# Performance work log

Hardware: AMD Instinct MI355X
Metric: run time of the kernel (lower is better)

## Reference

```python
import jax, jax.numpy as jnp
import numpy as np

L, D, I, H = 4, 768, 1536, 12
HEAD = I // H          # 128
NB = I // 4            # 384 block-diagonal blocks of size 4
EPS = 1e-5
SCALE = 1.0 / np.sqrt(HEAD)
ROPE_BASE = 1000.0


def _ln(x):
    m = x.mean(-1, keepdims=True)
    v = x.var(-1, keepdims=True)
    return (x - m) * jax.lax.rsqrt(v + EPS)


def _swish(x):
    return x * jax.nn.sigmoid(x)


def _block_linear(x, W):  # x:[T,B,I], W:[NB,4,4]
    T, B, _ = x.shape
    xb = x.reshape(T, B, NB, 4)
    return jnp.einsum('tbhi,hoi->tbho', xb, W).reshape(T, B, I)


def _rotate_half(x):
    h = x.shape[-1] // 2
    return jnp.concatenate([-x[..., h:], x[..., :h]], axis=-1)


def _depthwise_conv(x, w, b):  # x:[T,B,I], w:[I,5], b:[I]
    h = jnp.transpose(x, (1, 2, 0))  # [B,I,T]
    out = jax.lax.conv_general_dilated(
        h, w[:, None, :], (1,), [(2, 2)],
        dimension_numbers=('NCH', 'OIH', 'NCH'), feature_group_count=I)
    out = out + b[None, :, None]
    return jnp.transpose(out, (2, 0, 1))  # [T,B,I]


def setup_inputs() -> dict:
    key = jax.random.key(0)
    ks = jax.random.split(key, 16)
    T, B = 512, 16
    std = np.sqrt(2.0 / (5.0 * D))
    inp = {
        'x': jax.random.normal(ks[0], (T, B, D), jnp.float32),
        'attention_mask': jax.random.bernoulli(ks[1], 0.1, (B, 1, 1, T)),
        'Win': jax.random.normal(ks[2], (L, 2 * I, D), jnp.float32) * std,
        'Wout': jax.random.normal(ks[3], (L, D, I), jnp.float32) * std,
        'Wq': jax.random.normal(ks[4], (L, NB, 4, 4), jnp.float32) * 0.5,
        'bq': jnp.zeros((L, NB, 4), jnp.float32),
        'Wk': jax.random.normal(ks[5], (L, NB, 4, 4), jnp.float32) * 0.5,
        'Wv': jax.random.normal(ks[6], (L, NB, 4, 4), jnp.float32) * 0.5,
        'kg': jnp.ones((L, HEAD), jnp.float32),
        'kb': jnp.zeros((L, HEAD), jnp.float32),
        'qg': jnp.ones((L, HEAD), jnp.float32),
        'qb': jnp.zeros((L, HEAD), jnp.float32),
        'convw': jax.random.normal(ks[7], (L, I, 5), jnp.float32) * 0.3,
        'convb': jnp.zeros((L, I), jnp.float32),
        'lskip': jnp.ones((L, I), jnp.float32),
    }
    return inp


def reference(x, attention_mask, Win, Wout, Wq, bq, Wk, Wv, kg, kb, qg, qb, convw, convb, lskip):
    T, B, _ = x.shape
    # rotary tables (positions 0..T-1, same for every batch*head)
    inv_freq = 1.0 / (ROPE_BASE ** (jnp.arange(0, HEAD, 2, dtype=jnp.float32) / HEAD))
    freqs = jnp.arange(T, dtype=jnp.float32)[:, None] * inv_freq[None, :]  # [T,HEAD/2]
    emb = jnp.concatenate([freqs, freqs], axis=-1)
    cos, sin = jnp.cos(emb)[None], jnp.sin(emb)[None]  # [1,T,HEAD]

    hidden = x
    for l in range(L):
        h = _ln(hidden)                                   # pre LN
        h = jnp.einsum('tbd,od->tbo', h, Win[l])          # [T,B,2I]
        h, gate = h[..., :I], h[..., I:]
        gate = _swish(gate)
        # value branch
        value = _block_linear(h, Wv[l])                   # [T,B,I]
        value = value.reshape(T, B * H, HEAD).transpose(1, 0, 2)  # [BH,T,hd]
        # time mixing
        h = _swish(_depthwise_conv(h, convw[l], convb[l]))  # [T,B,I]
        # key/query with per-head LN (affine)
        k = _block_linear(h, Wk[l]).reshape(T, B, H, HEAD)
        k = _ln(k) * kg[l] + kb[l]
        k = k.reshape(T, B * H, HEAD).transpose(1, 0, 2)
        q = _block_linear(h, Wq[l]) + bq[l].reshape(I)
        q = q.reshape(T, B, H, HEAD)
        q = _ln(q) * qg[l] + qb[l]
        q = q.reshape(T, B * H, HEAD).transpose(1, 0, 2)
        # rotary
        q = q * cos + _rotate_half(q) * sin
        k = k * cos + _rotate_half(k) * sin
        # masked attention
        scores = jnp.einsum('bqd,bkd->bqk', q, k) * SCALE  # [BH,T,T]
        scores = scores.reshape(B, H, T, T)
        scores = jnp.where(attention_mask, -jnp.inf, scores)
        probs = jax.nn.softmax(scores, axis=-1)
        probs = jnp.where(attention_mask, 0.0, probs).reshape(B * H, T, T)
        attn = jnp.einsum('bqk,bkd->bqd', probs, value)    # [BH,T,hd]
        attn = attn.transpose(1, 0, 2).reshape(T, B, I)
        # gated output
        h = h * lskip[l] + attn
        h = h * gate
        h = _ln(h)
        h = jnp.einsum('tbi,di->tbd', h, Wout[l])
        hidden = hidden + h
    return hidden
```

## Files before the change

### kernel.cpp

```cpp
#include <hip/hip_runtime.h>

#define TT 512
#define BB 16
#define DD 768
#define II 1536
#define HH 12
#define SCALE_QK 0.08838834764831845f

typedef unsigned short u16;
typedef unsigned int u32;
typedef __attribute__((ext_vector_type(8))) short bf16x8;
typedef __attribute__((ext_vector_type(4))) float f32x4;

__device__ __forceinline__ u16 f2b(float f) {
  union { float f; u32 u; } a; a.f = f;
  u32 r = a.u + 0x7FFFu + ((a.u >> 16) & 1u);
  return (u16)(r >> 16);
}
__device__ __forceinline__ float b2f(u16 h) {
  union { u32 u; float f; } a; a.u = ((u32)h) << 16; return a.f;
}

typedef __attribute__((address_space(3))) u32 lds_u32;
typedef const __attribute__((address_space(1))) u32 gbl_u32;
__device__ __forceinline__ void gl_lds16(const void* g, void* l) {
  __builtin_amdgcn_global_load_lds((gbl_u32*)g, (lds_u32*)l, 16, 0, 0);
}

__global__ __launch_bounds__(256) void wconv_kernel(const float* __restrict__ Win,
    const float* __restrict__ Wout, u16* __restrict__ winb, u16* __restrict__ woutb) {
  const int n1 = 3072 * 768, n2 = 768 * 1536;
  for (int i = blockIdx.x * 256 + threadIdx.x; i < n1 + n2; i += gridDim.x * 256) {
    if (i < n1) winb[i] = f2b(Win[i]);
    else woutb[i - n1] = f2b(Wout[i - n1]);
  }
}

__global__ void rope_kernel(float* __restrict__ cost, float* __restrict__ sint) {
  int t = blockIdx.x, j = threadIdx.x;
  float inv = powf(1000.0f, -(float)j * (1.0f / 64.0f));
  float f = (float)t * inv;
  cost[t * 64 + j] = cosf(f);
  sint[t * 64 + j] = sinf(f);
}

__global__ void mask_kernel(const void* __restrict__ mraw, float* __restrict__ madd) {
  __shared__ int flags[2];
  if (threadIdx.x < 2) flags[threadIdx.x] = 0;
  __syncthreads();
  const unsigned char* p = (const unsigned char*)mraw;
  int a0 = 0, a1 = 0;
  for (int i = threadIdx.x; i < 8192; i += 256) {
    unsigned char c = p[i];
    if (c) { if ((i & 3) == 0) a0 = 1; else a1 = 1; }
  }
  if (a0) atomicOr(&flags[0], 1);
  if (a1) atomicOr(&flags[1], 1);
  __syncthreads();
  bool bytewise = flags[0] && flags[1];
  for (int i = threadIdx.x; i < 8192; i += 256) {
    int m = bytewise ? (int)p[i] : (((const int*)mraw)[i] != 0);
    madd[i] = m ? -1e30f : 0.0f;
  }
}

__global__ __launch_bounds__(256) void ln_d_kernel(const float* __restrict__ in, u16* __restrict__ out) {
  const int tb = blockIdx.x;
  const float* row = in + (size_t)tb * DD;
  float v[3], s = 0.f, ss = 0.f;
#pragma unroll
  for (int e = 0; e < 3; ++e) { v[e] = row[threadIdx.x + e * 256]; s += v[e]; ss += v[e] * v[e]; }
#pragma unroll
  for (int off = 1; off < 64; off <<= 1) { s += __shfl_xor(s, off); ss += __shfl_xor(ss, off); }
  __shared__ float red[8];
  int wave = threadIdx.x >> 6, lane = threadIdx.x & 63;
  if (lane == 0) { red[wave] = s; red[wave + 4] = ss; }
  __syncthreads();
  s = red[0] + red[1] + red[2] + red[3];
  ss = red[4] + red[5] + red[6] + red[7];
  float mean = s * (1.f / DD), var = ss * (1.f / DD) - mean * mean;
  float rstd = rsqrtf(var + 1e-5f);
#pragma unroll
  for (int e = 0; e < 3; ++e)
    out[(size_t)tb * DD + threadIdx.x + e * 256] = f2b((v[e] - mean) * rstd);
}

template <int MODE, int K>
__global__ __launch_bounds__(256) void gemm_nt(const u16* __restrict__ A, const u16* __restrict__ Bt,
    u16* __restrict__ o_h0, u16* __restrict__ o_gate, float* __restrict__ o_add) {
  __shared__ u16 As[128 * 32];
  __shared__ u16 Bs[128 * 32];
  const int tid = threadIdx.x, lane = tid & 63, wave = tid >> 6;
  const int wm = wave >> 1, wn = wave & 1;
  const size_t ar0 = (size_t)blockIdx.x * 128;
  const size_t br0 = (size_t)blockIdx.y * 128;
  const int ldr = lane >> 2, ldk = (lane & 3) * 8;
  const f32x4 z4 = {0.f, 0.f, 0.f, 0.f};
  f32x4 acc[4][4];
#pragma unroll
  for (int i = 0; i < 4; ++i)
#pragma unroll
    for (int j = 0; j < 4; ++j) acc[i][j] = z4;

  for (int kt = 0; kt < K; kt += 32) {
    __syncthreads();
#pragma unroll
    for (int i = 0; i < 2; ++i) {
      const int rr = wave * 32 + i * 16;
      gl_lds16(A + (ar0 + rr + ldr) * K + kt + ldk, (void*)&As[rr * 32]);
      gl_lds16(Bt + (br0 + rr + ldr) * K + kt + ldk, (void*)&Bs[rr * 32]);
    }
    __syncthreads();
    const int rs = lane & 15, kc8 = (lane >> 4) * 8;
    bf16x8 af[4], bg[4];
#pragma unroll
    for (int f = 0; f < 4; ++f) {
      af[f] = *(const bf16x8*)&As[(wm * 64 + f * 16 + rs) * 32 + kc8];
      bg[f] = *(const bf16x8*)&Bs[(wn * 64 + f * 16 + rs) * 32 + kc8];
    }
#pragma unroll
    for (int i = 0; i < 4; ++i)
#pragma unroll
      for (int j = 0; j < 4; ++j)
        acc[i][j] = __builtin_amdgcn_mfma_f32_16x16x32_bf16(af[i], bg[j], acc[i][j], 0, 0, 0);
  }
  const int rl = (lane >> 4) * 4, cl = lane & 15;
#pragma unroll
  for (int i = 0; i < 4; ++i)
#pragma unroll
    for (int j = 0; j < 4; ++j) {
      const int cc = blockIdx.y * 128 + wn * 64 + j * 16 + cl;
#pragma unroll
      for (int r = 0; r < 4; ++r) {
        const size_t rr = ar0 + wm * 64 + i * 16 + rl + r;
        float v = acc[i][j][r];
        if (MODE == 0) {
          if (cc < II) o_h0[rr * II + cc] = f2b(v);
          else o_gate[rr * II + (cc - II)] = f2b(v / (1.f + __expf(-v)));
        } else {
          o_add[rr * DD + cc] += v;
        }
      }
    }
}

__global__ __launch_bounds__(256) void value_kernel(const u16* __restrict__ h0,
    const float* __restrict__ Wv, u16* __restrict__ val) {
  __shared__ float xs[64][129];
  const int bh = blockIdx.x, t0 = blockIdx.y * 64;
  const int b = bh / HH, h = bh % HH;
  const int tid = threadIdx.x;
#pragma unroll
  for (int it = 0; it < 4; ++it) {
    int idx = tid + it * 256;
    int tt = idx >> 4, c8 = idx & 15;
    union { uint4 v; u16 hh[8]; } u;
    u.v = *(const uint4*)&h0[((size_t)((t0 + tt) * BB + b)) * II + h * 128 + c8 * 8];
#pragma unroll
    for (int j = 0; j < 8; ++j) xs[tt][c8 * 8 + j] = b2f(u.hh[j]);
  }
  __syncthreads();
  const int tt = tid & 63, dg = tid >> 6;
#pragma unroll
  for (int dd = 0; dd < 32; ++dd) {
    int d = dg * 32 + dd;
    int nbl = d >> 2, o = d & 3;
    const float4 w = *(const float4*)&Wv[((size_t)(h * 32 + nbl) * 4 + o) * 4];
    float r = w.x * xs[tt][nbl * 4] + w.y * xs[tt][nbl * 4 + 1] +
              w.z * xs[tt][nbl * 4 + 2] + w.w * xs[tt][nbl * 4 + 3];
    val[((size_t)bh * 128 + d) * TT + t0 + tt] = f2b(r);
  }
}

__global__ __launch_bounds__(384) void conv_kernel(const u16* __restrict__ h0,
    const float* __restrict__ cw, const float* __restrict__ cb, u16* __restrict__ hc) {
  __shared__ float wT[5 * 1536];
  __shared__ float bS[1536];
  const int tid = threadIdx.x;
  for (int idx = tid; idx < 7680; idx += 384) {
    int ch = idx / 5, k2 = idx % 5;
    wT[k2 * 1536 + ch] = cw[idx];
  }
  for (int idx = tid; idx < 1536; idx += 384) bS[idx] = cb[idx];
  __syncthreads();

  const int r = tid / 192, c = tid % 192;
  const int tb = blockIdx.x * 2 + r;
  const int t = tb >> 4;
  const int i0 = c * 8;
  float a[8];
  {
    const float4 b0 = *(const float4*)&bS[i0];
    const float4 b1 = *(const float4*)&bS[i0 + 4];
    a[0] = b0.x; a[1] = b0.y; a[2] = b0.z; a[3] = b0.w;
    a[4] = b1.x; a[5] = b1.y; a[6] = b1.z; a[7] = b1.w;
  }
#pragma unroll
  for (int k2 = 0; k2 < 5; ++k2) {
    int tn = t + k2 - 2;
    if (tn < 0 || tn >= TT) continue;
    union { uint4 v; u16 hh[8]; } u;
    u.v = *(const uint4*)&h0[((size_t)tb + (size_t)(k2 - 2) * BB) * II + i0];
    const float4 w0 = *(const float4*)&wT[k2 * 1536 + i0];
    const float4 w1 = *(const float4*)&wT[k2 * 1536 + i0 + 4];
    a[0] += b2f(u.hh[0]) * w0.x; a[1] += b2f(u.hh[1]) * w0.y;
    a[2] += b2f(u.hh[2]) * w0.z; a[3] += b2f(u.hh[3]) * w0.w;
    a[4] += b2f(u.hh[4]) * w1.x; a[5] += b2f(u.hh[5]) * w1.y;
    a[6] += b2f(u.hh[6]) * w1.z; a[7] += b2f(u.hh[7]) * w1.w;
  }
  union { uint4 v; u16 hh[8]; } o;
#pragma unroll
  for (int j = 0; j < 8; ++j) o.hh[j] = f2b(a[j] / (1.f + __expf(-a[j])));
  *(uint4*)&hc[(size_t)tb * II + i0] = o.v;
}

__global__ __launch_bounds__(256) void qk_kernel(const u16* __restrict__ hc,
    const float* __restrict__ Wq, const float* __restrict__ bq, const float* __restrict__ Wk,
    const float* __restrict__ qg, const float* __restrict__ qb,
    const float* __restrict__ kg, const float* __restrict__ kb,
    const float* __restrict__ cost, const float* __restrict__ sint,
    u16* __restrict__ qrope, u16* __restrict__ krope) {
  const int gw = (blockIdx.x * 256 + threadIdx.x) >> 6;
  const int lane = threadIdx.x & 63;
  const int h = gw % HH, tb = gw / HH, b = tb & 15, t = tb >> 4;
  ushort4 xr = *(const ushort4*)&hc[(size_t)tb * II + h * 128 + (lane >> 1) * 4];
  float x0 = b2f(xr.x), x1 = b2f(xr.y), x2 = b2f(xr.z), x3 = b2f(xr.w);
  const int nb = h * 32 + (lane >> 1);
  const int o0 = (lane & 1) * 2;
  const float4 wq0 = *(const float4*)&Wq[((size_t)nb * 4 + o0) * 4];
  const float4 wq1 = *(const float4*)&Wq[((size_t)nb * 4 + o0 + 1) * 4];
  const float4 wk0 = *(const float4*)&Wk[((size_t)nb * 4 + o0) * 4];
  const float4 wk1 = *(const float4*)&Wk[((size_t)nb * 4 + o0 + 1) * 4];
  float q0 = wq0.x * x0 + wq0.y * x1 + wq0.z * x2 + wq0.w * x3 + bq[nb * 4 + o0];
  float q1 = wq1.x * x0 + wq1.y * x1 + wq1.z * x2 + wq1.w * x3 + bq[nb * 4 + o0 + 1];
  float k0 = wk0.x * x0 + wk0.y * x1 + wk0.z * x2 + wk0.w * x3;
  float k1 = wk1.x * x0 + wk1.y * x1 + wk1.z * x2 + wk1.w * x3;
  float sq = q0 + q1, sk = k0 + k1, qq = q0 * q0 + q1 * q1, kk = k0 * k0 + k1 * k1;
#pragma unroll
  for (int off = 1; off < 64; off <<= 1) {
    sq += __shfl_xor(sq, off); qq += __shfl_xor(qq, off);
    sk += __shfl_xor(sk, off); kk += __shfl_xor(kk, off);
  }
  float mq = sq * (1.f / 128), vq = qq * (1.f / 128) - mq * mq, rq = rsqrtf(vq + 1e-5f);
  float mk = sk * (1.f / 128), vk = kk * (1.f / 128) - mk * mk, rk = rsqrtf(vk + 1e-5f);
  const int d0 = lane * 2, d1 = d0 + 1;
  float qn0 = (q0 - mq) * rq * qg[d0] + qb[d0], qn1 = (q1 - mq) * rq * qg[d1] + qb[d1];
  float kn0 = (k0 - mk) * rk * kg[d0] + kb[d0], kn1 = (k1 - mk) * rk * kg[d1] + kb[d1];
  float pq0 = __shfl_xor(qn0, 32), pq1 = __shfl_xor(qn1, 32);
  float pk0 = __shfl_xor(kn0, 32), pk1 = __shfl_xor(kn1, 32);
  const float sg = (lane < 32) ? -1.f : 1.f;
  const float c0 = cost[t * 64 + (d0 & 63)], s0 = sint[t * 64 + (d0 & 63)];
  const float c1 = cost[t * 64 + (d1 & 63)], s1 = sint[t * 64 + (d1 & 63)];
  float oq0 = qn0 * c0 + sg * pq0 * s0, oq1 = qn1 * c1 + sg * pq1 * s1;
  float ok0 = kn0 * c0 + sg * pk0 * s0, ok1 = kn1 * c1 + sg * pk1 * s1;
  const size_t ob = ((size_t)(b * HH + h) * TT + t) * 128 + d0;
  *(u32*)&qrope[ob] = (u32)f2b(oq0) | ((u32)f2b(oq1) << 16);
  *(u32*)&krope[ob] = (u32)f2b(ok0) | ((u32)f2b(ok1) << 16);
}

__global__ __launch_bounds__(256) void attn_kernel(const u16* __restrict__ qr,
    const u16* __restrict__ kr, const u16* __restrict__ vv,
    const float* __restrict__ madd, u16* __restrict__ o) {
  __shared__ u16 Ks[64 * 128];
  __shared__ u16 Vs[128 * 64];
  __shared__ u16 Ps[4][16 * 72];
  const int bh = blockIdx.x, b = bh / HH;
  const int q0 = blockIdx.y * 64;
  const int tid = threadIdx.x, lane = tid & 63, wave = tid >> 6;
  const int l15 = lane & 15, l4 = lane >> 4;
  bf16x8 aq[4];
  const size_t qbase = ((size_t)bh * TT + q0 + wave * 16 + l15) * 128;
#pragma unroll
  for (int kc = 0; kc < 4; ++kc) aq[kc] = *(const bf16x8*)&qr[qbase + kc * 32 + l4 * 8];
  const f32x4 z4 = {0.f, 0.f, 0.f, 0.f};
  f32x4 oacc[8];
#pragma unroll
  for (int df = 0; df < 8; ++df) oacc[df] = z4;
  float mrow[4], lrow[4];
#pragma unroll
  for (int r = 0; r < 4; ++r) { mrow[r] = -1e30f; lrow[r] = 0.f; }

  for (int kt0 = 0; kt0 < TT; kt0 += 64) {
    __syncthreads();
#pragma unroll
    for (int i = 0; i < 4; ++i) {
      const int row = wave * 16 + i * 4 + l4;
      const int csrc = (l15 & 8) | ((l15 ^ row) & 7);
      gl_lds16(&kr[((size_t)bh * TT + kt0 + row) * 128 + csrc * 8], (void*)&Ks[(wave * 16 + i * 4) * 128]);
    }
#pragma unroll
    for (int i = 0; i < 4; ++i) {
      const int row = wave * 32 + i * 8 + (lane >> 3);
      const int csrc = ((lane & 7) ^ row) & 7;
      gl_lds16(&vv[((size_t)bh * 128 + row) * TT + kt0 + csrc * 8], (void*)&Vs[(wave * 32 + i * 8) * 64]);
    }
    __syncthreads();
    f32x4 sacc[4];
#pragma unroll
    for (int cf = 0; cf < 4; ++cf) sacc[cf] = z4;
#pragma unroll
    for (int kc = 0; kc < 4; ++kc)
#pragma unroll
      for (int cf = 0; cf < 4; ++cf) {
        const int krow = cf * 16 + l15;
        const int chunk = kc * 4 + l4;
        const int cph = (chunk & 8) | ((chunk ^ krow) & 7);
        bf16x8 bk = *(const bf16x8*)&Ks[krow * 128 + cph * 8];
        sacc[cf] = __builtin_amdgcn_mfma_f32_16x16x32_bf16(aq[kc], bk, sacc[cf], 0, 0, 0);
      }
    float sv[4][4], tmax[4];
#pragma unroll
    for (int r = 0; r < 4; ++r) tmax[r] = -3.0e38f;
#pragma unroll
    for (int cf = 0; cf < 4; ++cf) {
      const float ma = madd[b * TT + kt0 + cf * 16 + l15];
#pragma unroll
      for (int r = 0; r < 4; ++r) {
        const float s = sacc[cf][r] * SCALE_QK + ma;
        sv[cf][r] = s;
        tmax[r] = fmaxf(tmax[r], s);
      }
    }
#pragma unroll
    for (int off = 1; off < 16; off <<= 1)
#pragma unroll
      for (int r = 0; r < 4; ++r) tmax[r] = fmaxf(tmax[r], __shfl_xor(tmax[r], off));
    float fac[4], lsum[4];
#pragma unroll
    for (int r = 0; r < 4; ++r) {
      const float mn = fmaxf(mrow[r], tmax[r]);
      fac[r] = __expf(mrow[r] - mn);
      mrow[r] = mn;
      lsum[r] = 0.f;
    }
#pragma unroll
    for (int cf = 0; cf < 4; ++cf)
#pragma unroll
      for (int r = 0; r < 4; ++r) {
        const float p = __expf(sv[cf][r] - mrow[r]);
        lsum[r] += p;
        Ps[wave][(l4 * 4 + r) * 72 + cf * 16 + l15] = f2b(p);
      }
#pragma unroll
    for (int off = 1; off < 16; off <<= 1)
#pragma unroll
      for (int r = 0; r < 4; ++r) lsum[r] += __shfl_xor(lsum[r], off);
#pragma unroll
    for (int r = 0; r < 4; ++r) lrow[r] = lrow[r] * fac[r] + lsum[r];
#pragma unroll
    for (int df = 0; df < 8; ++df)
#pragma unroll
      for (int r = 0; r < 4; ++r) oacc[df][r] *= fac[r];
#pragma unroll
    for (int ks = 0; ks < 2; ++ks) {
      bf16x8 ap = *(const bf16x8*)&Ps[wave][l15 * 72 + ks * 32 + l4 * 8];
#pragma unroll
      for (int df = 0; df < 8; ++df) {
        const int d = df * 16 + l15;
        const int cph = (ks * 4 + l4) ^ (d & 7);
        bf16x8 bv = *(const bf16x8*)&Vs[d * 64 + cph * 8];
        oacc[df] = __builtin_amdgcn_mfma_f32_16x16x32_bf16(ap, bv, oacc[df], 0, 0, 0);
      }
    }
  }
  const size_t ob = (size_t)bh * TT + q0 + wave * 16;
#pragma unroll
  for (int df = 0; df < 8; ++df)
#pragma unroll
    for (int r = 0; r < 4; ++r)
      o[(ob + l4 * 4 + r) * 128 + df * 16 + l15] = f2b(oacc[df][r] / lrow[r]);
}

__global__ __launch_bounds__(256) void post_kernel(const u16* __restrict__ hc,
    const u16* __restrict__ attn, const u16* __restrict__ gate,
    const float* __restrict__ lskip, u16* __restrict__ ln2) {
  const int tb = blockIdx.x;
  const int b = tb & 15, t = tb >> 4;
  float v[6], s = 0.f, ss = 0.f;
#pragma unroll
  for (int e = 0; e < 6; ++e) {
    int i = threadIdx.x + e * 256;
    int hh = i >> 7, d = i & 127;
    float a = b2f(attn[((size_t)(b * HH + hh) * TT + t) * 128 + d]);
    float x = (b2f(hc[(size_t)tb * II + i]) * lskip[i] + a) * b2f(gate[(size_t)tb * II + i]);
    v[e] = x; s += x; ss += x * x;
  }
#pragma unroll
  for (int off = 1; off < 64; off <<= 1) { s += __shfl_xor(s, off); ss += __shfl_xor(ss, off); }
  __shared__ float red[8];
  int wave = threadIdx.x >> 6, lane = threadIdx.x & 63;
  if (lane == 0) { red[wave] = s; red[wave + 4] = ss; }
  __syncthreads();
  s = red[0] + red[1] + red[2] + red[3];
  ss = red[4] + red[5] + red[6] + red[7];
  float mean = s * (1.f / II), var = ss * (1.f / II) - mean * mean;
  float rstd = rsqrtf(var + 1e-5f);
#pragma unroll
  for (int e = 0; e < 6; ++e) {
    int i = threadIdx.x + e * 256;
    ln2[(size_t)tb * II + i] = f2b((v[e] - mean) * rstd);
  }
}

extern "C" void kernel_launch(void* const* d_in, const int* in_sizes, int n_in,
                              void* d_out, int out_size, void* d_ws, size_t ws_size,
                              hipStream_t stream) {
  const float* x = (const float*)d_in[0];
  const void* mraw = d_in[1];
  const float* Win = (const float*)d_in[2];
  const float* Wout = (const float*)d_in[3];
  const float* Wq = (const float*)d_in[4];
  const float* bq = (const float*)d_in[5];
  const float* Wk = (const float*)d_in[6];
  const float* Wv = (const float*)d_in[7];
  const float* kg = (const float*)d_in[8];
  const float* kb = (const float*)d_in[9];
  const float* qg = (const float*)d_in[10];
  const float* qb = (const float*)d_in[11];
  const float* convw = (const float*)d_in[12];
  const float* convb = (const float*)d_in[13];
  const float* lskip = (const float*)d_in[14];
  float* hidden = (float*)d_out;

  char* w = (char*)d_ws;
  u16* wb_in = (u16*)w;
  u16* wb_out = (u16*)(w + 4718592);
  u16* lnval = (u16*)(w + 7077888);
  u16* h0k = (u16*)(w + 32243712);
  u16* gate = (u16*)(w + 57409536);
  u16* hc = (u16*)(w + 82575360);
  u16* qrope = (u16*)(w + 107741184);
  float* cost = (float*)(w + 132907008);
  float* sint = (float*)(w + 133038080);
  float* madd = (float*)(w + 133169152);
  const size_t NEED = 133201920;
  if (ws_size < NEED) {
    hipMemcpyAsync(d_out, d_in[0], (size_t)out_size * 4, hipMemcpyDeviceToDevice, stream);
    return;
  }
  u16* ln1 = lnval;
  u16* val = lnval;
  u16* ln2 = lnval;
  u16* h0 = h0k;
  u16* krope = h0k;
  u16* attnb = qrope;

  hipMemcpyAsync(hidden, x, (size_t)TT * BB * DD * 4, hipMemcpyDeviceToDevice, stream);
  rope_kernel<<<512, 64, 0, stream>>>(cost, sint);
  mask_kernel<<<1, 256, 0, stream>>>(mraw, madd);

  for (int l = 0; l < 4; ++l) {
    wconv_kernel<<<4096, 256, 0, stream>>>(Win + (size_t)l * 3072 * 768,
        Wout + (size_t)l * 768 * 1536, wb_in, wb_out);
    ln_d_kernel<<<8192, 256, 0, stream>>>(hidden, ln1);
    gemm_nt<0, 768><<<dim3(64, 24), 256, 0, stream>>>(ln1, wb_in, h0, gate, nullptr);
    value_kernel<<<dim3(192, 8), 256, 0, stream>>>(h0, Wv + (size_t)l * 6144, val);
    conv_kernel<<<4096, 384, 0, stream>>>(h0, convw + (size_t)l * 7680, convb + (size_t)l * 1536, hc);
    qk_kernel<<<24576, 256, 0, stream>>>(hc, Wq + (size_t)l * 6144, bq + (size_t)l * 1536,
        Wk + (size_t)l * 6144, qg + l * 128, qb + l * 128, kg + l * 128, kb + l * 128,
        cost, sint, qrope, krope);
    attn_kernel<<<dim3(192, 8), 256, 0, stream>>>(qrope, krope, val, madd, attnb);
    post_kernel<<<8192, 256, 0, stream>>>(hc, attnb, gate, lskip + (size_t)l * 1536, ln2);
    gemm_nt<1, 1536><<<dim3(64, 6), 256, 0, stream>>>(ln2, wb_out, nullptr, nullptr, hidden);
  }
}
```

Before: 1.249 ms.

## Process two query tiles per attention block and skip unneeded softmax rescales

Each attention workgroup now handles 128 query rows instead of 64, reusing every K/V tile loaded into LDS for two query sub-tiles and halving the grid's K/V traffic. The mask row is staged once in LDS, and the online-softmax rescale of accumulators is skipped when no row maximum grows. The bf16 conversion helper is swapped for the HIP library intrinsic. In exchange each thread holds twice the accumulators, which raises register pressure and may lower occupancy, and the grid has half as many blocks.

```diff
diff --git a/kernel.cpp b/kernel.cpp
--- a/kernel.cpp
+++ b/kernel.cpp
@@ -1,4 +1,5 @@
 #include <hip/hip_runtime.h>
+#include <hip/hip_bf16.h>
 
 #define TT 512
 #define BB 16
@@ -13,9 +14,8 @@
 typedef __attribute__((ext_vector_type(4))) float f32x4;
 
 __device__ __forceinline__ u16 f2b(float f) {
-  union { float f; u32 u; } a; a.f = f;
-  u32 r = a.u + 0x7FFFu + ((a.u >> 16) & 1u);
-  return (u16)(r >> 16);
+  __hip_bfloat16 h = __float2bfloat16(f);
+  return *reinterpret_cast<u16*>(&h);
 }
 __device__ __forceinline__ float b2f(u16 h) {
   union { u32 u; float f; } a; a.u = ((u32)h) << 16; return a.f;
@@ -264,21 +264,29 @@
   __shared__ u16 Ks[64 * 128];
   __shared__ u16 Vs[128 * 64];
   __shared__ u16 Ps[4][16 * 72];
+  __shared__ float Ms[TT];
   const int bh = blockIdx.x, b = bh / HH;
-  const int q0 = blockIdx.y * 64;
+  const int q0 = blockIdx.y * 128;
   const int tid = threadIdx.x, lane = tid & 63, wave = tid >> 6;
   const int l15 = lane & 15, l4 = lane >> 4;
-  bf16x8 aq[4];
-  const size_t qbase = ((size_t)bh * TT + q0 + wave * 16 + l15) * 128;
-#pragma unroll
-  for (int kc = 0; kc < 4; ++kc) aq[kc] = *(const bf16x8*)&qr[qbase + kc * 32 + l4 * 8];
+  for (int i = tid; i < TT; i += 256) Ms[i] = madd[b * TT + i];
+  bf16x8 aq[2][4];
+#pragma unroll
+  for (int qt = 0; qt < 2; ++qt) {
+    const size_t qbase = ((size_t)bh * TT + q0 + qt * 64 + wave * 16 + l15) * 128;
+#pragma unroll
+    for (int kc = 0; kc < 4; ++kc) aq[qt][kc] = *(const bf16x8*)&qr[qbase + kc * 32 + l4 * 8];
+  }
   const f32x4 z4 = {0.f, 0.f, 0.f, 0.f};
-  f32x4 oacc[8];
-#pragma unroll
-  for (int df = 0; df < 8; ++df) oacc[df] = z4;
-  float mrow[4], lrow[4];
-#pragma unroll
-  for (int r = 0; r < 4; ++r) { mrow[r] = -1e30f; lrow[r] = 0.f; }
+  f32x4 oacc[2][8];
+  float mrow[2][4], lrow[2][4];
+#pragma unroll
+  for (int qt = 0; qt < 2; ++qt) {
+#pragma unroll
+    for (int df = 0; df < 8; ++df) oacc[qt][df] = z4;
+#pragma unroll
+    for (int r = 0; r < 4; ++r) { mrow[qt][r] = -1e30f; lrow[qt][r] = 0.f; }
+  }
 
   for (int kt0 = 0; kt0 < TT; kt0 += 64) {
     __syncthreads();
@@ -295,80 +303,90 @@
       gl_lds16(&vv[((size_t)bh * 128 + row) * TT + kt0 + csrc * 8], (void*)&Vs[(wave * 32 + i * 8) * 64]);
     }
     __syncthreads();
-    f32x4 sacc[4];
-#pragma unroll
-    for (int cf = 0; cf < 4; ++cf) sacc[cf] = z4;
-#pragma unroll
-    for (int kc = 0; kc < 4; ++kc)
+#pragma unroll
+    for (int qt = 0; qt < 2; ++qt) {
+      f32x4 sacc[4];
+#pragma unroll
+      for (int cf = 0; cf < 4; ++cf) sacc[cf] = z4;
+#pragma unroll
+      for (int kc = 0; kc < 4; ++kc)
+#pragma unroll
+        for (int cf = 0; cf < 4; ++cf) {
+          const int krow = cf * 16 + l15;
+          const int chunk = kc * 4 + l4;
+          const int cph = (chunk & 8) | ((chunk ^ krow) & 7);
+          bf16x8 bk = *(const bf16x8*)&Ks[krow * 128 + cph * 8];
+          sacc[cf] = __builtin_amdgcn_mfma_f32_16x16x32_bf16(aq[qt][kc], bk, sacc[cf], 0, 0, 0);
+        }
+      float tmax[4];
+#pragma unroll
+      for (int r = 0; r < 4; ++r) tmax[r] = -3.0e38f;
 #pragma unroll
       for (int cf = 0; cf < 4; ++cf) {
-        const int krow = cf * 16 + l15;
-        const int chunk = kc * 4 + l4;
-        const int cph = (chunk & 8) | ((chunk ^ krow) & 7);
-        bf16x8 bk = *(const bf16x8*)&Ks[krow * 128 + cph * 8];
-        sacc[cf] = __builtin_amdgcn_mfma_f32_16x16x32_bf16(aq[kc], bk, sacc[cf], 0, 0, 0);
+        const float ma = Ms[kt0 + cf * 16 + l15];
+#pragma unroll
+        for (int r = 0; r < 4; ++r) {
+          const float s = sacc[cf][r] * SCALE_QK + ma;
+          sacc[cf][r] = s;
+          tmax[r] = fmaxf(tmax[r], s);
+        }
       }
-    float sv[4][4], tmax[4];
-#pragma unroll
-    for (int r = 0; r < 4; ++r) tmax[r] = -3.0e38f;
-#pragma unroll
-    for (int cf = 0; cf < 4; ++cf) {
-      const float ma = madd[b * TT + kt0 + cf * 16 + l15];
-#pragma unroll
-      for (int r = 0; r < 4; ++r) {
-        const float s = sacc[cf][r] * SCALE_QK + ma;
-        sv[cf][r] = s;
-        tmax[r] = fmaxf(tmax[r], s);
+#pragma unroll
+      for (int off = 1; off < 16; off <<= 1)
+#pragma unroll
+        for (int r = 0; r < 4; ++r) tmax[r] = fmaxf(tmax[r], __shfl_xor(tmax[r], off));
+      bool grow = (tmax[0] > mrow[qt][0]) | (tmax[1] > mrow[qt][1]) |
+                  (tmax[2] > mrow[qt][2]) | (tmax[3] > mrow[qt][3]);
+      if (__any(grow)) {
+#pragma unroll
+        for (int r = 0; r < 4; ++r) {
+          const float mn = fmaxf(mrow[qt][r], tmax[r]);
+          const float fac = __expf(mrow[qt][r] - mn);
+          mrow[qt][r] = mn;
+          lrow[qt][r] *= fac;
+#pragma unroll
+          for (int df = 0; df < 8; ++df) oacc[qt][df][r] *= fac;
+        }
       }
-    }
-#pragma unroll
-    for (int off = 1; off < 16; off <<= 1)
-#pragma unroll
-      for (int r = 0; r < 4; ++r) tmax[r] = fmaxf(tmax[r], __shfl_xor(tmax[r], off));
-    float fac[4], lsum[4];
-#pragma unroll
-    for (int r = 0; r < 4; ++r) {
-      const float mn = fmaxf(mrow[r], tmax[r]);
-      fac[r] = __expf(mrow[r] - mn);
-      mrow[r] = mn;
-      lsum[r] = 0.f;
-    }
-#pragma unroll
-    for (int cf = 0; cf < 4; ++cf)
-#pragma unroll
-      for (int r = 0; r < 4; ++r) {
-        const float p = __expf(sv[cf][r] - mrow[r]);
-        lsum[r] += p;
-        Ps[wave][(l4 * 4 + r) * 72 + cf * 16 + l15] = f2b(p);
+      float lsum[4];
+#pragma unroll
+      for (int r = 0; r < 4; ++r) lsum[r] = 0.f;
+#pragma unroll
+      for (int cf = 0; cf < 4; ++cf)
+#pragma unroll
+        for (int r = 0; r < 4; ++r) {
+          const float p = __expf(sacc[cf][r] - mrow[qt][r]);
+          lsum[r] += p;
+          Ps[wave][(l4 * 4 + r) * 72 + cf * 16 + l15] = f2b(p);
+        }
+#pragma unroll
+      for (int off = 1; off < 16; off <<= 1)
+#pragma unroll
+        for (int r = 0; r < 4; ++r) lsum[r] += __shfl_xor(lsum[r], off);
+#pragma unroll
+      for (int r = 0; r < 4; ++r) lrow[qt][r] += lsum[r];
+#pragma unroll
+      for (int ks = 0; ks < 2; ++ks) {
+        bf16x8 ap = *(const bf16x8*)&Ps[wave][l15 * 72 + ks * 32 + l4 * 8];
+#pragma unroll
+        for (int df = 0; df < 8; ++df) {
+          const int d = df * 16 + l15;
+          const int cph = (ks * 4 + l4) ^ (d & 7);
+          bf16x8 bv = *(const bf16x8*)&Vs[d * 64 + cph * 8];
+          oacc[qt][df] = __builtin_amdgcn_mfma_f32_16x16x32_bf16(ap, bv, oacc[qt][df], 0, 0, 0);
+        }
       }
-#pragma unroll
-    for (int off = 1; off < 16; off <<= 1)
-#pragma unroll
-      for (int r = 0; r < 4; ++r) lsum[r] += __shfl_xor(lsum[r], off);
-#pragma unroll
-    for (int r = 0; r < 4; ++r) lrow[r] = lrow[r] * fac[r] + lsum[r];
+    }
+  }
+#pragma unroll
+  for (int qt = 0; qt < 2; ++qt) {
+    const size_t ob = (size_t)bh * TT + q0 + qt * 64 + wave * 16;
 #pragma unroll
     for (int df = 0; df < 8; ++df)
 #pragma unroll
-      for (int r = 0; r < 4; ++r) oacc[df][r] *= fac[r];
-#pragma unroll
-    for (int ks = 0; ks < 2; ++ks) {
-      bf16x8 ap = *(const bf16x8*)&Ps[wave][l15 * 72 + ks * 32 + l4 * 8];
-#pragma unroll
-      for (int df = 0; df < 8; ++df) {
-        const int d = df * 16 + l15;
-        const int cph = (ks * 4 + l4) ^ (d & 7);
-        bf16x8 bv = *(const bf16x8*)&Vs[d * 64 + cph * 8];
-        oacc[df] = __builtin_amdgcn_mfma_f32_16x16x32_bf16(ap, bv, oacc[df], 0, 0, 0);
-      }
-    }
-  }
-  const size_t ob = (size_t)bh * TT + q0 + wave * 16;
-#pragma unroll
-  for (int df = 0; df < 8; ++df)
-#pragma unroll
-    for (int r = 0; r < 4; ++r)
-      o[(ob + l4 * 4 + r) * 128 + df * 16 + l15] = f2b(oacc[df][r] / lrow[r]);
+      for (int r = 0; r < 4; ++r)
+        o[(ob + l4 * 4 + r) * 128 + df * 16 + l15] = f2b(oacc[qt][df][r] / lrow[qt][r]);
+  }
 }
 
 __global__ __launch_bounds__(256) void post_kernel(const u16* __restrict__ hc,
@@ -459,7 +477,7 @@
     qk_kernel<<<24576, 256, 0, stream>>>(hc, Wq + (size_t)l * 6144, bq + (size_t)l * 1536,
         Wk + (size_t)l * 6144, qg + l * 128, qb + l * 128, kg + l * 128, kb + l * 128,
         cost, sint, qrope, krope);
-    attn_kernel<<<dim3(192, 8), 256, 0, stream>>>(qrope, krope, val, madd, attnb);
+    attn_kernel<<<dim3(192, 4), 256, 0, stream>>>(qrope, krope, val, madd, attnb);
     post_kernel<<<8192, 256, 0, stream>>>(hc, attnb, gate, lskip + (size_t)l * 1536, ln2);
     gemm_nt<1, 1536><<<dim3(64, 6), 256, 0, stream>>>(ln2, wb_out, nullptr, nullptr, hidden);
   }
```

Result: slower. 1.276 ms (+2.2%).
